# Performance work log

Measured on AMD Instinct MI355X. Metric: run time of the kernel, lower is better.

Reference implementation:

```python
import jax, jax.numpy as jnp
import numpy as np

HEAD_DIM = 128
NEG_INF = -1e10


def setup_inputs() -> dict:
    key = jax.random.key(0)
    k1, k2, k3, k4 = jax.random.split(key, 4)
    B, T, C, D = 4, 4096, 1024, HEAD_DIM
    x = jax.random.normal(k1, (B, T, C), dtype=jnp.float32)
    # nn.Linear(C, D, bias=False) weight is [D, C]; we store transposed [C, D]
    Wq = jax.random.normal(k2, (C, D), dtype=jnp.float32) * (1.0 / np.sqrt(C))
    Wk = jax.random.normal(k3, (C, D), dtype=jnp.float32) * (1.0 / np.sqrt(C))
    Wv = jax.random.normal(k4, (C, D), dtype=jnp.float32) * (1.0 / np.sqrt(C))
    return {"x": x, "Wq": Wq, "Wk": Wk, "Wv": Wv}


def reference(x, Wq, Wk, Wv):
    B, T, C = x.shape
    D = Wq.shape[1]
    Q = jnp.einsum("btc,cd->btd", x, Wq)
    K = jnp.einsum("btc,cd->btd", x, Wk)
    V = jnp.einsum("btc,cd->btd", x, Wv)
    scores = jnp.einsum("bqd,bkd->bqk", Q, K) * (1.0 / np.sqrt(D))
    causal = jnp.tril(jnp.ones((T, T), dtype=bool))  # [T, T]
    scores = jnp.where(causal, scores, NEG_INF)
    probs = jax.nn.softmax(scores, axis=-1)
    out = jnp.einsum("bqk,bkd->bqd", probs, V)
    return out
```

## Files before the change

### kernel.cpp

```cpp
#include <hip/hip_runtime.h>
#include <hip/hip_bf16.h>
#include <stdint.h>
#include <math.h>


typedef __attribute__((ext_vector_type(4))) float f32x4;
typedef __attribute__((ext_vector_type(8))) short bf16x8;
typedef __attribute__((ext_vector_type(4))) unsigned short u16x4;
typedef __attribute__((ext_vector_type(2))) unsigned int u32x2;

#define NBATCH 4
#define NT 4096
#define NC 1024
#define ND 128
#define BT (NBATCH * NT)
#define NSPLIT 8
#define KSPAN (NT / NSPLIT)

#define EXP2F(x) __builtin_amdgcn_exp2f(x)

__device__ __forceinline__ unsigned short f2bf(float f) {
  union { float f; uint32_t u; } v; v.f = f;
  uint32_t u = v.u;
  return (unsigned short)((u + 0x7FFFu + ((u >> 16) & 1u)) >> 16);
}

__device__ __forceinline__ float bf2f(unsigned short h) {
  union { uint32_t u; float f; } v; v.u = ((uint32_t)h) << 16;
  return v.f;
}

__device__ __forceinline__ bf16x8 cvt8(const f32x4 a0, const f32x4 a1) {
  bf16x8 r;
  r[0] = (short)f2bf(a0[0]); r[1] = (short)f2bf(a0[1]);
  r[2] = (short)f2bf(a0[2]); r[3] = (short)f2bf(a0[3]);
  r[4] = (short)f2bf(a1[0]); r[5] = (short)f2bf(a1[1]);
  r[6] = (short)f2bf(a1[2]); r[7] = (short)f2bf(a1[3]);
  return r;
}

__device__ __forceinline__ unsigned int cvtpk(float a, float b) {
  unsigned int r;
  asm("v_cvt_pk_bf16_f32 %0, %1, %2" : "=v"(r) : "v"(a), "v"(b));
  return r;
}

__device__ __forceinline__ void g2lds16(const void* g, void* l) {
  __builtin_amdgcn_global_load_lds(
      (const __attribute__((address_space(1))) unsigned int*)g,
      (__attribute__((address_space(3))) unsigned int*)l, 16, 0, 0);
}

__global__ void wcvt_kernel(const float* __restrict__ Wq, const float* __restrict__ Wk,
                            const float* __restrict__ Wv, unsigned short* __restrict__ Wt) {
  const float CK = 0.12751744f;
  int idx = blockIdx.x * blockDim.x + threadIdx.x;
  int m = idx >> 17;
  int r = idx & 131071;
  int d = r >> 10;
  int c = r & 1023;
  const float* W = (m == 0) ? Wq : (m == 1) ? Wk : Wv;
  float v = W[c * ND + d];
  if (m == 1) v *= CK;
  Wt[idx] = f2bf(v);
}

__global__ __launch_bounds__(256, 3)
void proj_kernel(const float* __restrict__ x, const unsigned short* __restrict__ Wt,
                 unsigned short* __restrict__ Qb, unsigned short* __restrict__ Kb,
                 unsigned short* __restrict__ Vt) {
  __shared__ char smem[2][16384];

  int w = threadIdx.x >> 6;
  int lane = threadIdx.x & 63;
  int r16 = lane & 15;
  int h4 = lane >> 4;
  int wm = w & 1;
  int wn = w >> 1;

  int mt = blockIdx.x & 255;
  int nt = blockIdx.x >> 8;

  const char* xg = (const char*)(x + (size_t)(mt * 64) * NC);
  const char* wg = (const char*)(Wt + (size_t)(nt * 128) * NC);

  f32x4 acc[2][4];
  #pragma unroll
  for (int m = 0; m < 2; ++m)
    #pragma unroll
    for (int n = 0; n < 4; ++n) acc[m][n] = (f32x4){0.f, 0.f, 0.f, 0.f};

  int cA0 = (w * 2 + 0) * 64 + lane;
  int cA1 = (w * 2 + 1) * 64 + lane;

  #define STAGE(buf, t)                                                          \
    {                                                                            \
      int c0 = (t) * 32;                                                         \
      {                                                                          \
        int c = cA0, row = c >> 3, s = c & 7;                                    \
        g2lds16(xg + (size_t)row * 4096 + c0 * 4 + ((s ^ (row & 7)) << 4),       \
                smem[buf] + (w * 2 + 0) * 1024);                                 \
      }                                                                          \
      {                                                                          \
        int c = cA1, row = c >> 3, s = c & 7;                                    \
        g2lds16(xg + (size_t)row * 4096 + c0 * 4 + ((s ^ (row & 7)) << 4),       \
                smem[buf] + (w * 2 + 1) * 1024);                                 \
      }                                                                          \
      {                                                                          \
        int c = cA0, row = c >> 2, s = c & 3;                                    \
        g2lds16(wg + (size_t)row * 2048 + c0 * 2 + ((s ^ (row & 3)) << 4),       \
                smem[buf] + 8192 + (w * 2 + 0) * 1024);                          \
      }                                                                          \
      {                                                                          \
        int c = cA1, row = c >> 2, s = c & 3;                                    \
        g2lds16(wg + (size_t)row * 2048 + c0 * 2 + ((s ^ (row & 3)) << 4),       \
                smem[buf] + 8192 + (w * 2 + 1) * 1024);                          \
      }                                                                          \
    }

  STAGE(0, 0);
  __syncthreads();

  for (int t = 0; t < 32; ++t) {
    int cur = t & 1;
    if (t + 1 < 32) STAGE(cur ^ 1, t + 1);

    bf16x8 af[2];
    #pragma unroll
    for (int m = 0; m < 2; ++m) {
      int row = wm * 32 + m * 16 + r16;
      f32x4 a0 = *(const f32x4*)(smem[cur] + row * 128 + (((h4 * 2) ^ (row & 7)) << 4));
      f32x4 a1 = *(const f32x4*)(smem[cur] + row * 128 + (((h4 * 2 + 1) ^ (row & 7)) << 4));
      af[m] = cvt8(a0, a1);
    }
    __builtin_amdgcn_s_setprio(1);
    #pragma unroll
    for (int n = 0; n < 4; ++n) {
      int brow = wn * 64 + n * 16 + r16;
      bf16x8 bfr = *(const bf16x8*)(smem[cur] + 8192 + brow * 64 + ((h4 ^ (brow & 3)) << 4));
      acc[0][n] = __builtin_amdgcn_mfma_f32_16x16x32_bf16(af[0], bfr, acc[0][n], 0, 0, 0);
      acc[1][n] = __builtin_amdgcn_mfma_f32_16x16x32_bf16(af[1], bfr, acc[1][n], 0, 0, 0);
    }
    __builtin_amdgcn_s_setprio(0);
    __syncthreads();
  }
  #undef STAGE

  if (nt < 2) {
    unsigned short* dst = (nt == 0) ? Qb : Kb;
    #pragma unroll
    for (int m = 0; m < 2; ++m) {
      int t0 = mt * 64 + wm * 32 + m * 16 + h4 * 4;
      #pragma unroll
      for (int n = 0; n < 4; ++n) {
        int d = wn * 64 + n * 16 + r16;
        #pragma unroll
        for (int r = 0; r < 4; ++r)
          dst[(size_t)(t0 + r) * ND + d] = f2bf(acc[m][n][r]);
      }
    }
  } else {
    #pragma unroll
    for (int m = 0; m < 2; ++m) {
      int t0 = mt * 64 + wm * 32 + m * 16 + h4 * 4;
      int b = t0 >> 12;
      int tl = t0 & (NT - 1);
      #pragma unroll
      for (int n = 0; n < 4; ++n) {
        int d = wn * 64 + n * 16 + r16;
        u16x4 pk;
        #pragma unroll
        for (int r = 0; r < 4; ++r) pk[r] = f2bf(acc[m][n][r]);
        *(u16x4*)(Vt + (size_t)b * (ND * NT) + (size_t)d * NT + tl) = pk;
      }
    }
  }
}

__global__ __launch_bounds__(256, 2)
void attn_kernel(const unsigned short* __restrict__ Qb,
                 const unsigned short* __restrict__ Kb,
                 const unsigned short* __restrict__ Vt,
                 unsigned short* __restrict__ Opart, float* __restrict__ Mpart,
                 float* __restrict__ Lpart) {
  __shared__ unsigned short kbuf[64 * 128];
  __shared__ unsigned short vbuf[128 * 64];
  __shared__ unsigned short plds[4][32][72];

  int wave = threadIdx.x >> 6;
  int lane = threadIdx.x & 63;
  int r16 = lane & 15;
  int h4 = lane >> 4;
  int h8 = h4 * 8;

  int l = blockIdx.x;
  int b = l & 3;
  int u = l >> 2;
  int a = (int)((sqrtf(2.0f * (float)u + 1.0f) - 1.0f) * 0.5f);
  if (a < 0) a = 0;
  while (2 * (a + 1) * (a + 2) <= u) ++a;
  while (a > 0 && 2 * a * (a + 1) > u) --a;
  int rem = u - 2 * a * (a + 1);
  int apl = a + 1;
  int rr = rem / apl;
  int s = rem - rr * apl;
  int qbt = 4 * a + rr;

  int qb0 = qbt * 128;
  int z = s;
  int kstart = s << 9;
  int kend = min(qb0 + 128, kstart + KSPAN);

  int q0 = qb0 + wave * 32;

  const unsigned short* Qbb = Qb + (size_t)b * NT * ND;
  const unsigned short* Kbb = Kb + (size_t)b * NT * ND;
  const unsigned short* Vtb = Vt + (size_t)b * ND * NT;

  bf16x8 qf[2][4];
  #pragma unroll
  for (int f = 0; f < 2; ++f)
    #pragma unroll
    for (int dc = 0; dc < 4; ++dc)
      qf[f][dc] = *(const bf16x8*)(Qbb + (size_t)(q0 + f * 16 + r16) * ND + dc * 32 + h8);

  f32x4 accO[2][8];
  #pragma unroll
  for (int f = 0; f < 2; ++f)
    #pragma unroll
    for (int i = 0; i < 8; ++i) accO[f][i] = (f32x4){0.f, 0.f, 0.f, 0.f};
  float mr[2] = {-1e30f, -1e30f};
  float lr[2] = {0.f, 0.f};

  for (int kv0 = kstart; kv0 < kend; kv0 += 64) {
    #pragma unroll
    for (int i = 0; i < 4; ++i) {
      int e = i * 256 + wave * 64 + lane;
      int krow = e >> 4, ks = e & 15;
      const char* gk = (const char*)(Kbb + (size_t)(kv0 + krow) * ND)
                       + ((ks * 16) ^ ((krow & 7) << 4));
      g2lds16(gk, (char*)kbuf + (size_t)(i * 256 + wave * 64) * 16);
    }
    #pragma unroll
    for (int i = 0; i < 4; ++i) {
      int e = i * 256 + wave * 64 + lane;
      int vrow = e >> 3, vs = e & 7;
      const char* gv = (const char*)(Vtb + (size_t)vrow * NT + kv0)
                       + ((vs * 16) ^ ((vrow & 7) << 4));
      g2lds16(gv, (char*)vbuf + (size_t)(i * 256 + wave * 64) * 16);
    }
    __syncthreads();

    if (kv0 < q0 + 32) {
      f32x4 sT[2][4];
      __builtin_amdgcn_s_setprio(1);
      #pragma unroll
      for (int kt = 0; kt < 4; ++kt) {
        sT[0][kt] = (f32x4){0.f, 0.f, 0.f, 0.f};
        sT[1][kt] = (f32x4){0.f, 0.f, 0.f, 0.f};
        int krow = kt * 16 + r16;
        #pragma unroll
        for (int dc = 0; dc < 4; ++dc) {
          int off = krow * 256 + ((dc * 64 + h4 * 16) ^ ((krow & 7) << 4));
          bf16x8 kf = *(const bf16x8*)((const char*)kbuf + off);
          sT[0][kt] = __builtin_amdgcn_mfma_f32_16x16x32_bf16(kf, qf[0][dc], sT[0][kt], 0, 0, 0);
          sT[1][kt] = __builtin_amdgcn_mfma_f32_16x16x32_bf16(kf, qf[1][dc], sT[1][kt], 0, 0, 0);
        }
      }
      __builtin_amdgcn_s_setprio(0);

      float pmax[2] = {-3e38f, -3e38f};
      if (kv0 + 63 <= q0) {
        #pragma unroll
        for (int kt = 0; kt < 4; ++kt)
          #pragma unroll
          for (int f = 0; f < 2; ++f)
            #pragma unroll
            for (int r = 0; r < 4; ++r) pmax[f] = fmaxf(pmax[f], sT[f][kt][r]);
      } else {
        #pragma unroll
        for (int kt = 0; kt < 4; ++kt) {
          int kb = kv0 + kt * 16 + h4 * 4;
          #pragma unroll
          for (int f = 0; f < 2; ++f) {
            int q = q0 + f * 16 + r16;
            #pragma unroll
            for (int r = 0; r < 4; ++r) {
              float v = (kb + r <= q) ? sT[f][kt][r] : -3e38f;
              sT[f][kt][r] = v;
              pmax[f] = fmaxf(pmax[f], v);
            }
          }
        }
      }

      bool grow = (pmax[0] > mr[0] + 11.0f) || (pmax[1] > mr[1] + 11.0f);
      if (__any(grow)) {
        float sf[2], sfa[2][4];
        #pragma unroll
        for (int f = 0; f < 2; ++f) {
          pmax[f] = fmaxf(pmax[f], __shfl_xor(pmax[f], 16, 64));
          pmax[f] = fmaxf(pmax[f], __shfl_xor(pmax[f], 32, 64));
          float mn = fmaxf(mr[f], pmax[f]);
          sf[f] = EXP2F(mr[f] - mn);
          mr[f] = mn;
          lr[f] *= sf[f];
        }
        #pragma unroll
        for (int f = 0; f < 2; ++f)
          #pragma unroll
          for (int r = 0; r < 4; ++r) sfa[f][r] = __shfl(sf[f], h4 * 4 + r, 64);
        #pragma unroll
        for (int f = 0; f < 2; ++f)
          #pragma unroll
          for (int dt = 0; dt < 8; ++dt) {
            #pragma unroll
            for (int r = 0; r < 4; ++r) accO[f][dt][r] *= sfa[f][r];
          }
      }

      #pragma unroll
      for (int f = 0; f < 2; ++f) {
        #pragma unroll
        for (int kt = 0; kt < 4; ++kt) {
          float p0 = EXP2F(sT[f][kt][0] - mr[f]);
          float p1 = EXP2F(sT[f][kt][1] - mr[f]);
          float p2 = EXP2F(sT[f][kt][2] - mr[f]);
          float p3 = EXP2F(sT[f][kt][3] - mr[f]);
          lr[f] += (p0 + p1) + (p2 + p3);
          u32x2 pk;
          pk[0] = cvtpk(p0, p1);
          pk[1] = cvtpk(p2, p3);
          *(u32x2*)&plds[wave][f * 16 + r16][kt * 16 + h4 * 4] = pk;
        }
      }

      __builtin_amdgcn_s_setprio(1);
      #pragma unroll
      for (int kc = 0; kc < 2; ++kc) {
        bf16x8 pf0 = *(const bf16x8*)(&plds[wave][r16][kc * 32 + h8]);
        bf16x8 pf1 = *(const bf16x8*)(&plds[wave][16 + r16][kc * 32 + h8]);
        #pragma unroll
        for (int dt = 0; dt < 8; ++dt) {
          int vrow = dt * 16 + r16;
          int off = vrow * 128 + ((kc * 64 + h4 * 16) ^ ((vrow & 7) << 4));
          bf16x8 vf = *(const bf16x8*)((const char*)vbuf + off);
          accO[0][dt] = __builtin_amdgcn_mfma_f32_16x16x32_bf16(pf0, vf, accO[0][dt], 0, 0, 0);
          accO[1][dt] = __builtin_amdgcn_mfma_f32_16x16x32_bf16(pf1, vf, accO[1][dt], 0, 0, 0);
        }
      }
      __builtin_amdgcn_s_setprio(0);
    }
    __syncthreads();
  }

  #pragma unroll
  for (int f = 0; f < 2; ++f) {
    lr[f] += __shfl_xor(lr[f], 16, 64);
    lr[f] += __shfl_xor(lr[f], 32, 64);
  }

  size_t pbase = ((size_t)z * NBATCH + b) * NT + q0;
  #pragma unroll
  for (int f = 0; f < 2; ++f)
    #pragma unroll
    for (int dt = 0; dt < 8; ++dt)
      #pragma unroll
      for (int r = 0; r < 4; ++r)
        Opart[(pbase + f * 16 + h4 * 4 + r) * ND + dt * 16 + r16] = f2bf(accO[f][dt][r]);
  if (h4 == 0) {
    #pragma unroll
    for (int f = 0; f < 2; ++f) {
      Mpart[pbase + f * 16 + r16] = mr[f];
      Lpart[pbase + f * 16 + r16] = lr[f];
    }
  }
}

__global__ void merge_kernel(const unsigned short* __restrict__ Opart,
                             const float* __restrict__ Mpart,
                             const float* __restrict__ Lpart, float* __restrict__ out) {
  int idx = blockIdx.x * blockDim.x + threadIdx.x;
  int bq = idx >> 4;
  int dg = idx & 15;
  int q = bq & (NT - 1);
  int nz = (q >> 9) + 1;

  float M = -3e38f;
  #pragma unroll
  for (int zz = 0; zz < NSPLIT; ++zz)
    if (zz < nz) M = fmaxf(M, Mpart[(size_t)zz * BT + bq]);

  float denom = 0.f;
  float o[8] = {0.f, 0.f, 0.f, 0.f, 0.f, 0.f, 0.f, 0.f};
  #pragma unroll
  for (int zz = 0; zz < NSPLIT; ++zz) {
    if (zz < nz) {
      float e = EXP2F(Mpart[(size_t)zz * BT + bq] - M);
      denom += e * Lpart[(size_t)zz * BT + bq];
      bf16x8 ov = *(const bf16x8*)(Opart + ((size_t)zz * BT + bq) * ND + dg * 8);
      #pragma unroll
      for (int j = 0; j < 8; ++j) o[j] += e * bf2f((unsigned short)ov[j]);
    }
  }
  float inv = 1.0f / denom;
  f32x4 o0, o1;
  #pragma unroll
  for (int j = 0; j < 4; ++j) { o0[j] = o[j] * inv; o1[j] = o[4 + j] * inv; }
  float* dst = out + (size_t)bq * ND + dg * 8;
  *(f32x4*)dst = o0;
  *(f32x4*)(dst + 4) = o1;
}

extern "C" void kernel_launch(void* const* d_in, const int* in_sizes, int n_in,
                              void* d_out, int out_size, void* d_ws, size_t ws_size,
                              hipStream_t stream) {
  const float* x  = (const float*)d_in[0];
  const float* Wq = (const float*)d_in[1];
  const float* Wk = (const float*)d_in[2];
  const float* Wv = (const float*)d_in[3];

  char* ws = (char*)d_ws;
  unsigned short* Qb = (unsigned short*)ws;
  unsigned short* Kb = (unsigned short*)(ws + 4194304);
  unsigned short* Vt = (unsigned short*)(ws + 8388608);
  unsigned short* Opart = (unsigned short*)(ws + 12582912);
  float* Mpart = (float*)(ws + 46137344);
  float* Lpart = (float*)(ws + 46661632);
  unsigned short* Wt = (unsigned short*)(ws + 12582912);

  hipLaunchKernelGGL(wcvt_kernel, dim3(1536), dim3(256), 0, stream, Wq, Wk, Wv, Wt);
  hipLaunchKernelGGL(proj_kernel, dim3(768), dim3(256), 0, stream, x, Wt, Qb, Kb, Vt);
  hipLaunchKernelGGL(attn_kernel, dim3(576), dim3(256), 0, stream,
                     Qb, Kb, Vt, Opart, Mpart, Lpart);
  hipLaunchKernelGGL(merge_kernel, dim3(BT * 16 / 256), dim3(256), 0, stream,
                     Opart, Mpart, Lpart, (float*)d_out);
}
```

Baseline: 79.74 us.

## Double-buffer K/V tiles via register prefetch and reswizzle LDS layouts

The attention loop now loads the next K/V tile from global memory into registers while the current tile is computed, then writes it into a second LDS buffer before the barrier. This replaces the direct global-to-LDS loads that stalled at a sync each iteration. The P staging buffer also gets an XOR-swizzled layout in place of padding, and the projection kernel's weight swizzle changes to reduce LDS bank conflicts. In exchange the kernel uses more LDS and registers, which may lower occupancy, and it leaves unused variables behind (eK, ksOffK, vsOffV).

```diff
diff --git a/kernel.cpp b/kernel.cpp
--- a/kernel.cpp
+++ b/kernel.cpp
@@ -108,12 +108,12 @@
       }                                                                          \
       {                                                                          \
         int c = cA0, row = c >> 2, s = c & 3;                                    \
-        g2lds16(wg + (size_t)row * 2048 + c0 * 2 + ((s ^ (row & 3)) << 4),       \
+        g2lds16(wg + (size_t)row * 2048 + c0 * 2 + ((s ^ ((row >> 1) & 3)) << 4),\
                 smem[buf] + 8192 + (w * 2 + 0) * 1024);                          \
       }                                                                          \
       {                                                                          \
         int c = cA1, row = c >> 2, s = c & 3;                                    \
-        g2lds16(wg + (size_t)row * 2048 + c0 * 2 + ((s ^ (row & 3)) << 4),       \
+        g2lds16(wg + (size_t)row * 2048 + c0 * 2 + ((s ^ ((row >> 1) & 3)) << 4),\
                 smem[buf] + 8192 + (w * 2 + 1) * 1024);                          \
       }                                                                          \
     }
@@ -137,7 +137,8 @@
     #pragma unroll
     for (int n = 0; n < 4; ++n) {
       int brow = wn * 64 + n * 16 + r16;
-      bf16x8 bfr = *(const bf16x8*)(smem[cur] + 8192 + brow * 64 + ((h4 ^ (brow & 3)) << 4));
+      bf16x8 bfr = *(const bf16x8*)(smem[cur] + 8192 + brow * 64 +
+                                    ((h4 ^ ((brow >> 1) & 3)) << 4));
       acc[0][n] = __builtin_amdgcn_mfma_f32_16x16x32_bf16(af[0], bfr, acc[0][n], 0, 0, 0);
       acc[1][n] = __builtin_amdgcn_mfma_f32_16x16x32_bf16(af[1], bfr, acc[1][n], 0, 0, 0);
     }
@@ -183,15 +184,16 @@
                  const unsigned short* __restrict__ Vt,
                  unsigned short* __restrict__ Opart, float* __restrict__ Mpart,
                  float* __restrict__ Lpart) {
-  __shared__ unsigned short kbuf[64 * 128];
-  __shared__ unsigned short vbuf[128 * 64];
-  __shared__ unsigned short plds[4][32][72];
+  __shared__ unsigned short kbuf[2][64 * 128];
+  __shared__ unsigned short vbuf[2][128 * 64];
+  __shared__ unsigned short plds[4][32 * 64];
 
   int wave = threadIdx.x >> 6;
   int lane = threadIdx.x & 63;
   int r16 = lane & 15;
   int h4 = lane >> 4;
   int h8 = h4 * 8;
+  int a7 = r16 & 7;
 
   int l = blockIdx.x;
   int b = l & 3;
@@ -217,6 +219,17 @@
   const unsigned short* Kbb = Kb + (size_t)b * NT * ND;
   const unsigned short* Vtb = Vt + (size_t)b * ND * NT;
 
+  int eK[4], ksOffK[4], eV[4], vsOffV[4];
+  #pragma unroll
+  for (int i = 0; i < 4; ++i) {
+    int e = i * 256 + wave * 64 + lane;
+    eK[i] = e;
+    int krow = e >> 4, ks = e & 15;
+    ksOffK[i] = krow;
+    eV[i] = ((ks * 16) ^ ((krow & 7) << 4));
+    (void)vsOffV;
+  }
+
   bf16x8 qf[2][4];
   #pragma unroll
   for (int f = 0; f < 2; ++f)
@@ -232,24 +245,41 @@
   float mr[2] = {-1e30f, -1e30f};
   float lr[2] = {0.f, 0.f};
 
+  #define LOAD_TILE(kv, kreg, vreg)                                             \
+    {                                                                           \
+      _Pragma("unroll")                                                         \
+      for (int i = 0; i < 4; ++i) {                                             \
+        int e = i * 256 + wave * 64 + lane;                                     \
+        int krow = e >> 4, ks = e & 15;                                         \
+        kreg[i] = *(const bf16x8*)((const char*)(Kbb + (size_t)((kv) + krow) * ND) \
+                                   + ((ks * 16) ^ ((krow & 7) << 4)));          \
+        int vrow = e >> 3, vs = e & 7;                                          \
+        vreg[i] = *(const bf16x8*)((const char*)(Vtb + (size_t)vrow * NT + (kv))\
+                                   + ((vs * 16) ^ ((vrow & 7) << 4)));          \
+      }                                                                         \
+    }
+  #define WRITE_TILE(bi, kreg, vreg)                                            \
+    {                                                                           \
+      _Pragma("unroll")                                                         \
+      for (int i = 0; i < 4; ++i) {                                             \
+        int e = i * 256 + wave * 64 + lane;                                     \
+        *(bf16x8*)((char*)kbuf[bi] + (size_t)e * 16) = kreg[i];                 \
+        *(bf16x8*)((char*)vbuf[bi] + (size_t)e * 16) = vreg[i];                 \
+      }                                                                         \
+    }
+
+  {
+    bf16x8 kreg[4], vreg[4];
+    LOAD_TILE(kstart, kreg, vreg);
+    WRITE_TILE(0, kreg, vreg);
+  }
+  __syncthreads();
+
+  int cur = 0;
   for (int kv0 = kstart; kv0 < kend; kv0 += 64) {
-    #pragma unroll
-    for (int i = 0; i < 4; ++i) {
-      int e = i * 256 + wave * 64 + lane;
-      int krow = e >> 4, ks = e & 15;
-      const char* gk = (const char*)(Kbb + (size_t)(kv0 + krow) * ND)
-                       + ((ks * 16) ^ ((krow & 7) << 4));
-      g2lds16(gk, (char*)kbuf + (size_t)(i * 256 + wave * 64) * 16);
-    }
-    #pragma unroll
-    for (int i = 0; i < 4; ++i) {
-      int e = i * 256 + wave * 64 + lane;
-      int vrow = e >> 3, vs = e & 7;
-      const char* gv = (const char*)(Vtb + (size_t)vrow * NT + kv0)
-                       + ((vs * 16) ^ ((vrow & 7) << 4));
-      g2lds16(gv, (char*)vbuf + (size_t)(i * 256 + wave * 64) * 16);
-    }
-    __syncthreads();
+    bf16x8 kreg[4], vreg[4];
+    bool have_next = (kv0 + 64 < kend);
+    if (have_next) LOAD_TILE(kv0 + 64, kreg, vreg);
 
     if (kv0 < q0 + 32) {
       f32x4 sT[2][4];
@@ -262,7 +292,7 @@
         #pragma unroll
         for (int dc = 0; dc < 4; ++dc) {
           int off = krow * 256 + ((dc * 64 + h4 * 16) ^ ((krow & 7) << 4));
-          bf16x8 kf = *(const bf16x8*)((const char*)kbuf + off);
+          bf16x8 kf = *(const bf16x8*)((const char*)kbuf[cur] + off);
           sT[0][kt] = __builtin_amdgcn_mfma_f32_16x16x32_bf16(kf, qf[0][dc], sT[0][kt], 0, 0, 0);
           sT[1][kt] = __builtin_amdgcn_mfma_f32_16x16x32_bf16(kf, qf[1][dc], sT[1][kt], 0, 0, 0);
         }
@@ -321,6 +351,7 @@
 
       #pragma unroll
       for (int f = 0; f < 2; ++f) {
+        int row = f * 16 + r16;
         #pragma unroll
         for (int kt = 0; kt < 4; ++kt) {
           float p0 = EXP2F(sT[f][kt][0] - mr[f]);
@@ -331,28 +362,35 @@
           u32x2 pk;
           pk[0] = cvtpk(p0, p1);
           pk[1] = cvtpk(p2, p3);
-          *(u32x2*)&plds[wave][f * 16 + r16][kt * 16 + h4 * 4] = pk;
+          int slot = (2 * kt + (h4 >> 1)) ^ a7;
+          *(u32x2*)&plds[wave][row * 64 + slot * 8 + (h4 & 1) * 4] = pk;
         }
       }
 
       __builtin_amdgcn_s_setprio(1);
       #pragma unroll
       for (int kc = 0; kc < 2; ++kc) {
-        bf16x8 pf0 = *(const bf16x8*)(&plds[wave][r16][kc * 32 + h8]);
-        bf16x8 pf1 = *(const bf16x8*)(&plds[wave][16 + r16][kc * 32 + h8]);
+        int sl = ((4 * kc + h4) ^ a7) * 8;
+        bf16x8 pf0 = *(const bf16x8*)(&plds[wave][r16 * 64 + sl]);
+        bf16x8 pf1 = *(const bf16x8*)(&plds[wave][(16 + r16) * 64 + sl]);
         #pragma unroll
         for (int dt = 0; dt < 8; ++dt) {
           int vrow = dt * 16 + r16;
           int off = vrow * 128 + ((kc * 64 + h4 * 16) ^ ((vrow & 7) << 4));
-          bf16x8 vf = *(const bf16x8*)((const char*)vbuf + off);
+          bf16x8 vf = *(const bf16x8*)((const char*)vbuf[cur] + off);
           accO[0][dt] = __builtin_amdgcn_mfma_f32_16x16x32_bf16(pf0, vf, accO[0][dt], 0, 0, 0);
           accO[1][dt] = __builtin_amdgcn_mfma_f32_16x16x32_bf16(pf1, vf, accO[1][dt], 0, 0, 0);
         }
       }
       __builtin_amdgcn_s_setprio(0);
     }
+
+    if (have_next) WRITE_TILE(cur ^ 1, kreg, vreg);
     __syncthreads();
-  }
+    cur ^= 1;
+  }
+  #undef LOAD_TILE
+  #undef WRITE_TILE
 
   #pragma unroll
   for (int f = 0; f < 2; ++f) {
```

New measurement: 80.69 us. Within noise of the previous version (+1.2%).

## Fuse Q/K/V projection tiles into one block to reuse x tile

Applied to the files above, without the earlier changes.

The projection kernel now computes all 384 output columns (Q, K and V) for each 64-row tile of x in a single 512-thread block, instead of three separate blocks per row tile. This means x is read from global memory and converted to bf16 once rather than three times. The trade-offs are a larger shared-memory footprint per block (64KB), more accumulators per wave, fewer blocks (256), and a changed LDS swizzle for the weight tile.

```diff
diff --git a/kernel.cpp b/kernel.cpp
--- a/kernel.cpp
+++ b/kernel.cpp
@@ -65,56 +65,44 @@
   Wt[idx] = f2bf(v);
 }
 
-__global__ __launch_bounds__(256, 3)
+__global__ __launch_bounds__(512, 2)
 void proj_kernel(const float* __restrict__ x, const unsigned short* __restrict__ Wt,
                  unsigned short* __restrict__ Qb, unsigned short* __restrict__ Kb,
                  unsigned short* __restrict__ Vt) {
-  __shared__ char smem[2][16384];
-
-  int w = threadIdx.x >> 6;
-  int lane = threadIdx.x & 63;
+  __shared__ char smem[2][32768];
+
+  int tid = threadIdx.x;
+  int w = tid >> 6;
+  int lane = tid & 63;
   int r16 = lane & 15;
   int h4 = lane >> 4;
-  int wm = w & 1;
-  int wn = w >> 1;
-
-  int mt = blockIdx.x & 255;
-  int nt = blockIdx.x >> 8;
+  int wm = w >> 2;
+  int wn = w & 3;
+
+  int mt = blockIdx.x;
 
   const char* xg = (const char*)(x + (size_t)(mt * 64) * NC);
-  const char* wg = (const char*)(Wt + (size_t)(nt * 128) * NC);
-
-  f32x4 acc[2][4];
+  const char* wg = (const char*)Wt;
+
+  f32x4 acc[2][6];
   #pragma unroll
   for (int m = 0; m < 2; ++m)
     #pragma unroll
-    for (int n = 0; n < 4; ++n) acc[m][n] = (f32x4){0.f, 0.f, 0.f, 0.f};
-
-  int cA0 = (w * 2 + 0) * 64 + lane;
-  int cA1 = (w * 2 + 1) * 64 + lane;
+    for (int n = 0; n < 6; ++n) acc[m][n] = (f32x4){0.f, 0.f, 0.f, 0.f};
 
   #define STAGE(buf, t)                                                          \
     {                                                                            \
       int c0 = (t) * 32;                                                         \
       {                                                                          \
-        int c = cA0, row = c >> 3, s = c & 7;                                    \
+        int c = tid, row = c >> 3, s = c & 7;                                    \
         g2lds16(xg + (size_t)row * 4096 + c0 * 4 + ((s ^ (row & 7)) << 4),       \
-                smem[buf] + (w * 2 + 0) * 1024);                                 \
+                smem[buf] + w * 1024);                                           \
       }                                                                          \
-      {                                                                          \
-        int c = cA1, row = c >> 3, s = c & 7;                                    \
-        g2lds16(xg + (size_t)row * 4096 + c0 * 4 + ((s ^ (row & 7)) << 4),       \
-                smem[buf] + (w * 2 + 1) * 1024);                                 \
-      }                                                                          \
-      {                                                                          \
-        int c = cA0, row = c >> 2, s = c & 3;                                    \
-        g2lds16(wg + (size_t)row * 2048 + c0 * 2 + ((s ^ (row & 3)) << 4),       \
-                smem[buf] + 8192 + (w * 2 + 0) * 1024);                          \
-      }                                                                          \
-      {                                                                          \
-        int c = cA1, row = c >> 2, s = c & 3;                                    \
-        g2lds16(wg + (size_t)row * 2048 + c0 * 2 + ((s ^ (row & 3)) << 4),       \
-                smem[buf] + 8192 + (w * 2 + 1) * 1024);                          \
+      _Pragma("unroll")                                                          \
+      for (int j = 0; j < 3; ++j) {                                              \
+        int c = j * 512 + tid, row = c >> 2, s = c & 3;                          \
+        g2lds16(wg + (size_t)row * 2048 + c0 * 2 + ((s ^ ((row >> 1) & 3)) << 4),\
+                smem[buf] + 8192 + j * 8192 + w * 1024);                         \
       }                                                                          \
     }
 
@@ -135,9 +123,10 @@
     }
     __builtin_amdgcn_s_setprio(1);
     #pragma unroll
-    for (int n = 0; n < 4; ++n) {
-      int brow = wn * 64 + n * 16 + r16;
-      bf16x8 bfr = *(const bf16x8*)(smem[cur] + 8192 + brow * 64 + ((h4 ^ (brow & 3)) << 4));
+    for (int n = 0; n < 6; ++n) {
+      int brow = wn * 96 + n * 16 + r16;
+      bf16x8 bfr = *(const bf16x8*)(smem[cur] + 8192 + brow * 64 +
+                                    ((h4 ^ ((brow >> 1) & 3)) << 4));
       acc[0][n] = __builtin_amdgcn_mfma_f32_16x16x32_bf16(af[0], bfr, acc[0][n], 0, 0, 0);
       acc[1][n] = __builtin_amdgcn_mfma_f32_16x16x32_bf16(af[1], bfr, acc[1][n], 0, 0, 0);
     }
@@ -146,28 +135,22 @@
   }
   #undef STAGE
 
-  if (nt < 2) {
-    unsigned short* dst = (nt == 0) ? Qb : Kb;
-    #pragma unroll
-    for (int m = 0; m < 2; ++m) {
-      int t0 = mt * 64 + wm * 32 + m * 16 + h4 * 4;
-      #pragma unroll
-      for (int n = 0; n < 4; ++n) {
-        int d = wn * 64 + n * 16 + r16;
+  #pragma unroll
+  for (int m = 0; m < 2; ++m) {
+    int t0 = mt * 64 + wm * 32 + m * 16 + h4 * 4;
+    #pragma unroll
+    for (int n = 0; n < 6; ++n) {
+      int col0 = wn * 96 + n * 16;
+      int matq = col0 >> 7;
+      int d = (col0 & 127) + r16;
+      if (matq < 2) {
+        unsigned short* dst = (matq == 0) ? Qb : Kb;
         #pragma unroll
         for (int r = 0; r < 4; ++r)
           dst[(size_t)(t0 + r) * ND + d] = f2bf(acc[m][n][r]);
-      }
-    }
-  } else {
-    #pragma unroll
-    for (int m = 0; m < 2; ++m) {
-      int t0 = mt * 64 + wm * 32 + m * 16 + h4 * 4;
-      int b = t0 >> 12;
-      int tl = t0 & (NT - 1);
-      #pragma unroll
-      for (int n = 0; n < 4; ++n) {
-        int d = wn * 64 + n * 16 + r16;
+      } else {
+        int b = t0 >> 12;
+        int tl = t0 & (NT - 1);
         u16x4 pk;
         #pragma unroll
         for (int r = 0; r < 4; ++r) pk[r] = f2bf(acc[m][n][r]);
@@ -430,7 +413,7 @@
   unsigned short* Wt = (unsigned short*)(ws + 12582912);
 
   hipLaunchKernelGGL(wcvt_kernel, dim3(1536), dim3(256), 0, stream, Wq, Wk, Wv, Wt);
-  hipLaunchKernelGGL(proj_kernel, dim3(768), dim3(256), 0, stream, x, Wt, Qb, Kb, Vt);
+  hipLaunchKernelGGL(proj_kernel, dim3(256), dim3(512), 0, stream, x, Wt, Qb, Kb, Vt);
   hipLaunchKernelGGL(attn_kernel, dim3(576), dim3(256), 0, stream,
                      Qb, Kb, Vt, Opart, Mpart, Lpart);
   hipLaunchKernelGGL(merge_kernel, dim3(BT * 16 / 256), dim3(256), 0, stream,
```

New measurement: 85.54 us. 1.07x slower.

## Double KV tile to 128 rows and swizzle LDS for weights and P

Applied to the files above, without the earlier changes.

The attention kernel now stages 128 K/V rows per iteration and processes them as two 64-row halves, which halves the number of block-wide barriers and load phases per KV span. The P staging buffer is reorganized into an XOR-swizzled 64-wide layout to avoid LDS bank conflicts, and the projection kernel's weight tile swizzle changes from row&3 to (row>>1)&3. LDS use rises to roughly 80 KB per block, which may limit the two-blocks-per-CU occupancy the launch bounds ask for.

```diff
diff --git a/kernel.cpp b/kernel.cpp
--- a/kernel.cpp
+++ b/kernel.cpp
@@ -108,12 +108,12 @@
       }                                                                          \
       {                                                                          \
         int c = cA0, row = c >> 2, s = c & 3;                                    \
-        g2lds16(wg + (size_t)row * 2048 + c0 * 2 + ((s ^ (row & 3)) << 4),       \
+        g2lds16(wg + (size_t)row * 2048 + c0 * 2 + ((s ^ ((row >> 1) & 3)) << 4),\
                 smem[buf] + 8192 + (w * 2 + 0) * 1024);                          \
       }                                                                          \
       {                                                                          \
         int c = cA1, row = c >> 2, s = c & 3;                                    \
-        g2lds16(wg + (size_t)row * 2048 + c0 * 2 + ((s ^ (row & 3)) << 4),       \
+        g2lds16(wg + (size_t)row * 2048 + c0 * 2 + ((s ^ ((row >> 1) & 3)) << 4),\
                 smem[buf] + 8192 + (w * 2 + 1) * 1024);                          \
       }                                                                          \
     }
@@ -137,7 +137,8 @@
     #pragma unroll
     for (int n = 0; n < 4; ++n) {
       int brow = wn * 64 + n * 16 + r16;
-      bf16x8 bfr = *(const bf16x8*)(smem[cur] + 8192 + brow * 64 + ((h4 ^ (brow & 3)) << 4));
+      bf16x8 bfr = *(const bf16x8*)(smem[cur] + 8192 + brow * 64 +
+                                    ((h4 ^ ((brow >> 1) & 3)) << 4));
       acc[0][n] = __builtin_amdgcn_mfma_f32_16x16x32_bf16(af[0], bfr, acc[0][n], 0, 0, 0);
       acc[1][n] = __builtin_amdgcn_mfma_f32_16x16x32_bf16(af[1], bfr, acc[1][n], 0, 0, 0);
     }
@@ -183,15 +184,16 @@
                  const unsigned short* __restrict__ Vt,
                  unsigned short* __restrict__ Opart, float* __restrict__ Mpart,
                  float* __restrict__ Lpart) {
-  __shared__ unsigned short kbuf[64 * 128];
-  __shared__ unsigned short vbuf[128 * 64];
-  __shared__ unsigned short plds[4][32][72];
+  __shared__ unsigned short kbuf[128 * 128];
+  __shared__ unsigned short vbuf[128 * 128];
+  __shared__ unsigned short plds[4][2048];
 
   int wave = threadIdx.x >> 6;
   int lane = threadIdx.x & 63;
   int r16 = lane & 15;
   int h4 = lane >> 4;
   int h8 = h4 * 8;
+  int a7 = r16 & 7;
 
   int l = blockIdx.x;
   int b = l & 3;
@@ -232,124 +234,132 @@
   float mr[2] = {-1e30f, -1e30f};
   float lr[2] = {0.f, 0.f};
 
-  for (int kv0 = kstart; kv0 < kend; kv0 += 64) {
-    #pragma unroll
-    for (int i = 0; i < 4; ++i) {
+  for (int kv0 = kstart; kv0 < kend; kv0 += 128) {
+    #pragma unroll
+    for (int i = 0; i < 8; ++i) {
       int e = i * 256 + wave * 64 + lane;
       int krow = e >> 4, ks = e & 15;
       const char* gk = (const char*)(Kbb + (size_t)(kv0 + krow) * ND)
                        + ((ks * 16) ^ ((krow & 7) << 4));
-      g2lds16(gk, (char*)kbuf + (size_t)(i * 256 + wave * 64) * 16);
-    }
-    #pragma unroll
-    for (int i = 0; i < 4; ++i) {
+      g2lds16(gk, (char*)kbuf + (size_t)e * 16);
+    }
+    #pragma unroll
+    for (int i = 0; i < 8; ++i) {
       int e = i * 256 + wave * 64 + lane;
-      int vrow = e >> 3, vs = e & 7;
+      int vrow = e >> 4, vs = e & 15;
       const char* gv = (const char*)(Vtb + (size_t)vrow * NT + kv0)
                        + ((vs * 16) ^ ((vrow & 7) << 4));
-      g2lds16(gv, (char*)vbuf + (size_t)(i * 256 + wave * 64) * 16);
+      g2lds16(gv, (char*)vbuf + (size_t)e * 16);
     }
     __syncthreads();
 
-    if (kv0 < q0 + 32) {
-      f32x4 sT[2][4];
-      __builtin_amdgcn_s_setprio(1);
-      #pragma unroll
-      for (int kt = 0; kt < 4; ++kt) {
-        sT[0][kt] = (f32x4){0.f, 0.f, 0.f, 0.f};
-        sT[1][kt] = (f32x4){0.f, 0.f, 0.f, 0.f};
-        int krow = kt * 16 + r16;
-        #pragma unroll
-        for (int dc = 0; dc < 4; ++dc) {
-          int off = krow * 256 + ((dc * 64 + h4 * 16) ^ ((krow & 7) << 4));
-          bf16x8 kf = *(const bf16x8*)((const char*)kbuf + off);
-          sT[0][kt] = __builtin_amdgcn_mfma_f32_16x16x32_bf16(kf, qf[0][dc], sT[0][kt], 0, 0, 0);
-          sT[1][kt] = __builtin_amdgcn_mfma_f32_16x16x32_bf16(kf, qf[1][dc], sT[1][kt], 0, 0, 0);
-        }
-      }
-      __builtin_amdgcn_s_setprio(0);
-
-      float pmax[2] = {-3e38f, -3e38f};
-      if (kv0 + 63 <= q0) {
-        #pragma unroll
-        for (int kt = 0; kt < 4; ++kt)
-          #pragma unroll
-          for (int f = 0; f < 2; ++f)
-            #pragma unroll
-            for (int r = 0; r < 4; ++r) pmax[f] = fmaxf(pmax[f], sT[f][kt][r]);
-      } else {
+    #pragma unroll
+    for (int half = 0; half < 2; ++half) {
+      int kvh = kv0 + half * 64;
+      if (kvh < q0 + 32) {
+        f32x4 sT[2][4];
+        __builtin_amdgcn_s_setprio(1);
         #pragma unroll
         for (int kt = 0; kt < 4; ++kt) {
-          int kb = kv0 + kt * 16 + h4 * 4;
-          #pragma unroll
-          for (int f = 0; f < 2; ++f) {
-            int q = q0 + f * 16 + r16;
+          sT[0][kt] = (f32x4){0.f, 0.f, 0.f, 0.f};
+          sT[1][kt] = (f32x4){0.f, 0.f, 0.f, 0.f};
+          int krow = half * 64 + kt * 16 + r16;
+          #pragma unroll
+          for (int dc = 0; dc < 4; ++dc) {
+            int off = krow * 256 + ((dc * 64 + h4 * 16) ^ ((krow & 7) << 4));
+            bf16x8 kf = *(const bf16x8*)((const char*)kbuf + off);
+            sT[0][kt] = __builtin_amdgcn_mfma_f32_16x16x32_bf16(kf, qf[0][dc], sT[0][kt], 0, 0, 0);
+            sT[1][kt] = __builtin_amdgcn_mfma_f32_16x16x32_bf16(kf, qf[1][dc], sT[1][kt], 0, 0, 0);
+          }
+        }
+        __builtin_amdgcn_s_setprio(0);
+
+        float pmax[2] = {-3e38f, -3e38f};
+        if (kvh + 63 <= q0) {
+          #pragma unroll
+          for (int kt = 0; kt < 4; ++kt)
             #pragma unroll
-            for (int r = 0; r < 4; ++r) {
-              float v = (kb + r <= q) ? sT[f][kt][r] : -3e38f;
-              sT[f][kt][r] = v;
-              pmax[f] = fmaxf(pmax[f], v);
+            for (int f = 0; f < 2; ++f)
+              #pragma unroll
+              for (int r = 0; r < 4; ++r) pmax[f] = fmaxf(pmax[f], sT[f][kt][r]);
+        } else {
+          #pragma unroll
+          for (int kt = 0; kt < 4; ++kt) {
+            int kb = kvh + kt * 16 + h4 * 4;
+            #pragma unroll
+            for (int f = 0; f < 2; ++f) {
+              int q = q0 + f * 16 + r16;
+              #pragma unroll
+              for (int r = 0; r < 4; ++r) {
+                float v = (kb + r <= q) ? sT[f][kt][r] : -3e38f;
+                sT[f][kt][r] = v;
+                pmax[f] = fmaxf(pmax[f], v);
+              }
             }
           }
         }
-      }
-
-      bool grow = (pmax[0] > mr[0] + 11.0f) || (pmax[1] > mr[1] + 11.0f);
-      if (__any(grow)) {
-        float sf[2], sfa[2][4];
+
+        bool grow = (pmax[0] > mr[0] + 11.0f) || (pmax[1] > mr[1] + 11.0f);
+        if (__any(grow)) {
+          float sf[2], sfa[2][4];
+          #pragma unroll
+          for (int f = 0; f < 2; ++f) {
+            pmax[f] = fmaxf(pmax[f], __shfl_xor(pmax[f], 16, 64));
+            pmax[f] = fmaxf(pmax[f], __shfl_xor(pmax[f], 32, 64));
+            float mn = fmaxf(mr[f], pmax[f]);
+            sf[f] = EXP2F(mr[f] - mn);
+            mr[f] = mn;
+            lr[f] *= sf[f];
+          }
+          #pragma unroll
+          for (int f = 0; f < 2; ++f)
+            #pragma unroll
+            for (int r = 0; r < 4; ++r) sfa[f][r] = __shfl(sf[f], h4 * 4 + r, 64);
+          #pragma unroll
+          for (int f = 0; f < 2; ++f)
+            #pragma unroll
+            for (int dt = 0; dt < 8; ++dt) {
+              #pragma unroll
+              for (int r = 0; r < 4; ++r) accO[f][dt][r] *= sfa[f][r];
+            }
+        }
+
         #pragma unroll
         for (int f = 0; f < 2; ++f) {
-          pmax[f] = fmaxf(pmax[f], __shfl_xor(pmax[f], 16, 64));
-          pmax[f] = fmaxf(pmax[f], __shfl_xor(pmax[f], 32, 64));
-          float mn = fmaxf(mr[f], pmax[f]);
-          sf[f] = EXP2F(mr[f] - mn);
-          mr[f] = mn;
-          lr[f] *= sf[f];
+          int row = f * 16 + r16;
+          #pragma unroll
+          for (int kt = 0; kt < 4; ++kt) {
+            float p0 = EXP2F(sT[f][kt][0] - mr[f]);
+            float p1 = EXP2F(sT[f][kt][1] - mr[f]);
+            float p2 = EXP2F(sT[f][kt][2] - mr[f]);
+            float p3 = EXP2F(sT[f][kt][3] - mr[f]);
+            lr[f] += (p0 + p1) + (p2 + p3);
+            u32x2 pk;
+            pk[0] = cvtpk(p0, p1);
+            pk[1] = cvtpk(p2, p3);
+            int slot = (2 * kt + (h4 >> 1)) ^ a7;
+            *(u32x2*)&plds[wave][row * 64 + slot * 8 + (h4 & 1) * 4] = pk;
+          }
         }
+
+        __builtin_amdgcn_s_setprio(1);
         #pragma unroll
-        for (int f = 0; f < 2; ++f)
-          #pragma unroll
-          for (int r = 0; r < 4; ++r) sfa[f][r] = __shfl(sf[f], h4 * 4 + r, 64);
-        #pragma unroll
-        for (int f = 0; f < 2; ++f)
+        for (int kc = 0; kc < 2; ++kc) {
+          int sl = ((4 * kc + h4) ^ a7) * 8;
+          bf16x8 pf0 = *(const bf16x8*)(&plds[wave][r16 * 64 + sl]);
+          bf16x8 pf1 = *(const bf16x8*)(&plds[wave][(16 + r16) * 64 + sl]);
           #pragma unroll
           for (int dt = 0; dt < 8; ++dt) {
-            #pragma unroll
-            for (int r = 0; r < 4; ++r) accO[f][dt][r] *= sfa[f][r];
+            int vrow = dt * 16 + r16;
+            int voff = vrow * 256 +
+                       ((half * 128 + kc * 64 + h4 * 16) ^ ((vrow & 7) << 4));
+            bf16x8 vf = *(const bf16x8*)((const char*)vbuf + voff);
+            accO[0][dt] = __builtin_amdgcn_mfma_f32_16x16x32_bf16(pf0, vf, accO[0][dt], 0, 0, 0);
+            accO[1][dt] = __builtin_amdgcn_mfma_f32_16x16x32_bf16(pf1, vf, accO[1][dt], 0, 0, 0);
           }
+        }
+        __builtin_amdgcn_s_setprio(0);
       }
-
-      #pragma unroll
-      for (int f = 0; f < 2; ++f) {
-        #pragma unroll
-        for (int kt = 0; kt < 4; ++kt) {
-          float p0 = EXP2F(sT[f][kt][0] - mr[f]);
-          float p1 = EXP2F(sT[f][kt][1] - mr[f]);
-          float p2 = EXP2F(sT[f][kt][2] - mr[f]);
-          float p3 = EXP2F(sT[f][kt][3] - mr[f]);
-          lr[f] += (p0 + p1) + (p2 + p3);
-          u32x2 pk;
-          pk[0] = cvtpk(p0, p1);
-          pk[1] = cvtpk(p2, p3);
-          *(u32x2*)&plds[wave][f * 16 + r16][kt * 16 + h4 * 4] = pk;
-        }
-      }
-
-      __builtin_amdgcn_s_setprio(1);
-      #pragma unroll
-      for (int kc = 0; kc < 2; ++kc) {
-        bf16x8 pf0 = *(const bf16x8*)(&plds[wave][r16][kc * 32 + h8]);
-        bf16x8 pf1 = *(const bf16x8*)(&plds[wave][16 + r16][kc * 32 + h8]);
-        #pragma unroll
-        for (int dt = 0; dt < 8; ++dt) {
-          int vrow = dt * 16 + r16;
-          int off = vrow * 128 + ((kc * 64 + h4 * 16) ^ ((vrow & 7) << 4));
-          bf16x8 vf = *(const bf16x8*)((const char*)vbuf + off);
-          accO[0][dt] = __builtin_amdgcn_mfma_f32_16x16x32_bf16(pf0, vf, accO[0][dt], 0, 0, 0);
-          accO[1][dt] = __builtin_amdgcn_mfma_f32_16x16x32_bf16(pf1, vf, accO[1][dt], 0, 0, 0);
-        }
-      }
-      __builtin_amdgcn_s_setprio(0);
     }
     __syncthreads();
   }
```

After: 78.83 us. Within noise of the previous version (-1.1%).
